# Optimization experiments

Hardware: AMD Instinct MI355X
Metric: run time of the kernel (lower is better)

## Reference

```python
import jax, jax.numpy as jnp
import numpy as np

B, IN, OUT, E, H, K = 8192, 1024, 256, 16, 512, 3
EPS = 1e-10


def setup_inputs() -> dict:
    key = jax.random.key(0)
    ks = jax.random.split(key, 5)
    scaled = lambda k, shape, fan: jax.random.normal(k, shape, jnp.float32) / np.sqrt(fan)
    return {
        "x": jax.random.normal(ks[0], (B, IN), jnp.float32),
        # torch init is zeros for w_gate (degenerate ties); use small random for a meaningful reference
        "w_gate": jax.random.normal(ks[1], (IN, E), jnp.float32) * 0.02,
        "W1": scaled(ks[2], (E, IN, H), IN),
        "b1": jnp.zeros((E, H), jnp.float32),
        "W2": scaled(ks[3], (E, H, OUT), H),
        "b2": jnp.zeros((E, OUT), jnp.float32),
    }


def _cv_squared(v):
    # torch .var() is unbiased (ddof=1)
    return jnp.var(v, ddof=1) / (jnp.mean(v) ** 2 + EPS)


def reference(x, w_gate, W1, b1, W2, b2):
    # --- top-k gating (eval mode: clean logits, no noise) ---
    logits = x @ w_gate                                   # [B, E]
    top_vals, top_idx = jax.lax.top_k(logits, K)          # [B, K]
    top_gates = jax.nn.softmax(top_vals, axis=-1)         # softmax over selected k
    rows = jnp.arange(logits.shape[0])[:, None]
    gates = jnp.zeros_like(logits).at[rows, top_idx].set(top_gates)  # sparse gates [B, E]

    # --- load-balancing loss ---
    importance = gates.sum(0)
    load = (gates > 0).sum(0).astype(jnp.float32)         # _gates_to_load (eval path)
    loss = _cv_squared(importance) + _cv_squared(load)

    # --- experts (MLP stand-in; dense compute, sparse combine via zero gates) ---
    h = jax.nn.relu(jnp.einsum('bi,eih->beh', x, W1) + b1)  # [B, E, H]
    expert_out = jnp.einsum('beh,eho->beo', h, W2) + b2     # [B, E, OUT]

    # combine: equivalent to SparseDispatcher gather/split/scatter-add with gate weighting
    y = jnp.einsum('be,beo->bo', gates, expert_out)         # [B, OUT]
    return y, loss
```

## Files before the change

### kernel.cpp

```cpp
#include <hip/hip_runtime.h>

#define B_ 8192
#define IN_ 1024
#define OUT_ 256
#define E_ 16
#define KTOP 3
#define H_ 512
#define MAXSLOTS 26624
#define NTILES 208
#define HBLK 16

typedef __bf16 bf16;
typedef __bf16 bf16x4 __attribute__((ext_vector_type(4)));
typedef __bf16 bf16x8 __attribute__((ext_vector_type(8)));
typedef float f32x4 __attribute__((ext_vector_type(4)));

__device__ __forceinline__ void async16(const bf16* g, bf16* l) {
    __builtin_amdgcn_global_load_lds(
        (const __attribute__((address_space(1))) void*)g,
        (__attribute__((address_space(3))) void*)l,
        16, 0, 0);
}

__global__ __launch_bounds__(256) void k_setup(
    const float* __restrict__ W1, bf16* __restrict__ w1t,
    const float* __restrict__ W2, bf16* __restrict__ w2t,
    int* __restrict__ row_ids, const float* __restrict__ wg, float* __restrict__ wgT,
    bf16* __restrict__ zero_row, int* __restrict__ tile_expert) {
    int bx = blockIdx.x;
    int t = threadIdx.x;
    if (bx >= 2560) {
        if (bx < 2664) {
            row_ids[(bx - 2560) * 256 + t] = -1;
        } else if (bx < 2728) {
            int id = (bx - 2664) * 256 + t;
            int e = id >> 10, j = id & 1023;
            wgT[id] = wg[j * E_ + e];
        } else {
#pragma unroll
            for (int i = 0; i < 4; i++) zero_row[t * 4 + i] = (bf16)0.f;
            if (t < NTILES) tile_expert[t] = -1;
        }
        return;
    }
    __shared__ float tile[64][65];
    const float* in; bf16* out; int Kd, Nd, e, tk, tn;
    if (bx < 2048) {
        in = W1; out = w1t; Kd = IN_; Nd = H_;
        e = bx >> 7; int tt = bx & 127; tk = tt >> 3; tn = tt & 7;
    } else {
        int b2x = bx - 2048;
        in = W2; out = w2t; Kd = H_; Nd = OUT_;
        e = b2x >> 5; int tt = b2x & 31; tk = tt >> 2; tn = tt & 3;
    }
    int r = t >> 6, c = t & 63;
    const float* src = in + ((size_t)e * Kd + tk * 64) * Nd + (size_t)tn * 64;
#pragma unroll
    for (int i = 0; i < 16; i++) {
        int rr = r + i * 4;
        tile[rr][c] = src[(size_t)rr * Nd + c];
    }
    __syncthreads();
    bf16* dst = out + ((size_t)e * Nd + tn * 64) * Kd + (size_t)tk * 64;
#pragma unroll
    for (int i = 0; i < 16; i++) {
        int rr = r + i * 4;
        dst[(size_t)rr * Kd + c] = (bf16)tile[c][rr];
    }
}

__global__ __launch_bounds__(256) void k_gating(
    const float* __restrict__ x, const float* __restrict__ wgT,
    bf16* __restrict__ xbf, int* __restrict__ top_idx, float* __restrict__ top_gate) {
    int t = threadIdx.x;
    int row = blockIdx.x * 4 + (t >> 6);
    int lane = t & 63;
    float acc[16];
#pragma unroll
    for (int e = 0; e < 16; e++) acc[e] = 0.f;
    const float4* x4p = (const float4*)(x + (size_t)row * IN_);
    const float4* w4 = (const float4*)wgT;
#pragma unroll
    for (int it = 0; it < 4; it++) {
        int j0 = it * 64 + lane;
        float4 xv = x4p[j0];
        bf16x4 xb;
        xb[0] = (bf16)xv.x; xb[1] = (bf16)xv.y; xb[2] = (bf16)xv.z; xb[3] = (bf16)xv.w;
        *(bf16x4*)(xbf + (size_t)row * IN_ + j0 * 4) = xb;
#pragma unroll
        for (int e = 0; e < 16; e++) {
            float4 wv = w4[e * 256 + j0];
            acc[e] += xv.x * wv.x + xv.y * wv.y + xv.z * wv.z + xv.w * wv.w;
        }
    }
#pragma unroll
    for (int e = 0; e < 16; e++) {
#pragma unroll
        for (int s = 32; s > 0; s >>= 1) acc[e] += __shfl_xor(acc[e], s, 64);
    }
    if (lane == 0) {
        float v[16];
#pragma unroll
        for (int e = 0; e < 16; e++) v[e] = acc[e];
        int idx[KTOP];
        float val[KTOP];
#pragma unroll
        for (int k = 0; k < KTOP; k++) {
            int best = 0;
            float bv = v[0];
            for (int e = 1; e < 16; e++) {
                if (v[e] > bv) { bv = v[e]; best = e; }
            }
            idx[k] = best; val[k] = bv; v[best] = -1e30f;
        }
        float e1 = __expf(val[1] - val[0]);
        float e2 = __expf(val[2] - val[0]);
        float inv = 1.f / (1.f + e1 + e2);
        float g[KTOP] = {inv, e1 * inv, e2 * inv};
#pragma unroll
        for (int k = 0; k < KTOP; k++) {
            top_idx[row * KTOP + k] = idx[k];
            top_gate[row * KTOP + k] = g[k];
        }
    }
}

__global__ __launch_bounds__(256) void k_hist(
    const int* __restrict__ top_idx, int* __restrict__ partial) {
    __shared__ int wcnt[4][16];
    int t = threadIdx.x;
    int w = t >> 6, lane = t & 63;
    int blk = blockIdx.x;
    int cnt[16];
#pragma unroll
    for (int k = 0; k < 16; k++) cnt[k] = 0;
#pragma unroll
    for (int j = 0; j < 6; j++) {
        int e = top_idx[blk * 1536 + j * 256 + t];
#pragma unroll
        for (int k = 0; k < 16; k++)
            cnt[k] += (int)__popcll(__ballot(e == k));
    }
    if (lane == 0) {
#pragma unroll
        for (int k = 0; k < 16; k++) wcnt[w][k] = cnt[k];
    }
    __syncthreads();
    if (t < 16) partial[blk * 16 + t] = wcnt[0][t] + wcnt[1][t] + wcnt[2][t] + wcnt[3][t];
}

__global__ __launch_bounds__(256) void k_scan(
    const int* __restrict__ partial, int* __restrict__ counts,
    int* __restrict__ tile_expert, int* __restrict__ gbase) {
    __shared__ int sp[HBLK * 16];
    __shared__ int soff[16];
    int t = threadIdx.x;
    sp[t] = partial[t];
    __syncthreads();
    if (t < 16) {
        int s = 0;
#pragma unroll
        for (int b = 0; b < HBLK; b++) s += sp[b * 16 + t];
        counts[t] = s;
    }
    __syncthreads();
    if (t == 0) {
        int off = 0;
        for (int e = 0; e < E_; e++) {
            int c = 0;
#pragma unroll
            for (int b = 0; b < HBLK; b++) c += sp[b * 16 + e];
            soff[e] = off;
            int pd = (c + 127) & ~127;
            int t0 = off >> 7, t1 = (off + pd) >> 7;
            for (int tt = t0; tt < t1; ++tt) tile_expert[tt] = e;
            off += pd;
        }
    }
    __syncthreads();
    {
        int b = t >> 4, e = t & 15;
        int s = soff[e];
        for (int bp = 0; bp < b; bp++) s += sp[bp * 16 + e];
        gbase[t] = s;
    }
}

__global__ __launch_bounds__(256) void k_scatter(
    const int* __restrict__ top_idx, const float* __restrict__ top_gate,
    const int* __restrict__ gbase,
    int* __restrict__ row_ids, int* __restrict__ rowslot,
    float* __restrict__ partial_imp) {
    __shared__ int lcnt[16];
    __shared__ float limp[16];
    int t = threadIdx.x;
    int blk = blockIdx.x;
    if (t < 16) { lcnt[t] = 0; limp[t] = 0.f; }
    __syncthreads();
#pragma unroll
    for (int j = 0; j < 6; j++) {
        int gid = blk * 1536 + j * 256 + t;
        int e = top_idx[gid];
        float g = top_gate[gid];
        int rank = atomicAdd(&lcnt[e], 1);
        atomicAdd(&limp[e], g);
        int slot = gbase[blk * 16 + e] + rank;
        row_ids[slot] = gid / KTOP;
        rowslot[gid] = slot;
    }
    __syncthreads();
    if (t < 16) partial_imp[blk * 16 + t] = limp[t];
}

__global__ __launch_bounds__(256) void k_gemm1(
    const bf16* __restrict__ xbf, const bf16* __restrict__ w1t,
    const float* __restrict__ b1, const int* __restrict__ row_ids,
    const int* __restrict__ tile_expert, const bf16* __restrict__ zero_row,
    bf16* __restrict__ h) {
    int e = tile_expert[blockIdx.y];
    if (e < 0) return;
    int slot_base = blockIdx.y * 128;
    int nbase = blockIdx.x * 128;
    __shared__ __align__(16) bf16 As[128 * 64];
    __shared__ __align__(16) bf16 Bs[128 * 64];
    int t = threadIdx.x;
    int rmod = (t >> 3) & 7;
    int cglob = (t & 7) ^ rmod;
    const bf16* gA[4];
    const bf16* gB[4];
#pragma unroll
    for (int j = 0; j < 4; j++) {
        int m = j * 32 + (t >> 3);
        int rid = row_ids[slot_base + m];
        gA[j] = ((rid >= 0) ? xbf + (size_t)rid * IN_ : zero_row) + cglob * 8;
        gB[j] = w1t + ((size_t)e * H_ + nbase + m) * IN_ + cglob * 8;
    }
    int w = t >> 6, lane = t & 63;
    int wm = (w >> 1) * 64, wn = (w & 1) * 64;
    int lm = lane & 15, lq = lane >> 4;
    f32x4 acc[4][4] = {};
    for (int k0 = 0; k0 < IN_; k0 += 64) {
#pragma unroll
        for (int j = 0; j < 4; j++) {
            async16(gA[j] + k0, As + (j * 256 + t) * 8);
            async16(gB[j] + k0, Bs + (j * 256 + t) * 8);
        }
        __syncthreads();
        const bf16x8* Av = (const bf16x8*)As;
        const bf16x8* Bv = (const bf16x8*)Bs;
#pragma unroll
        for (int ks = 0; ks < 2; ks++) {
            int kc = ks * 4 + lq;
            bf16x8 af[4], bfv[4];
#pragma unroll
            for (int i = 0; i < 4; i++) {
                int row = wm + i * 16 + lm;
                af[i] = Av[row * 8 + (kc ^ (row & 7))];
            }
#pragma unroll
            for (int i = 0; i < 4; i++) {
                int row = wn + i * 16 + lm;
                bfv[i] = Bv[row * 8 + (kc ^ (row & 7))];
            }
#pragma unroll
            for (int mi = 0; mi < 4; mi++)
#pragma unroll
                for (int ni = 0; ni < 4; ni++)
                    acc[mi][ni] = __builtin_amdgcn_mfma_f32_16x16x32_bf16(af[mi], bfv[ni], acc[mi][ni], 0, 0, 0);
        }
        __syncthreads();
    }
#pragma unroll
    for (int mi = 0; mi < 4; mi++) {
#pragma unroll
        for (int ni = 0; ni < 4; ni++) {
            int colg = nbase + wn + ni * 16 + lm;
            float bias = b1[e * H_ + colg];
#pragma unroll
            for (int r = 0; r < 4; r++) {
                int rowl = wm + mi * 16 + lq * 4 + r;
                float v = acc[mi][ni][r] + bias;
                v = v > 0.f ? v : 0.f;
                h[(size_t)(slot_base + rowl) * H_ + colg] = (bf16)v;
            }
        }
    }
}

__global__ __launch_bounds__(256) void k_gemm2(
    const bf16* __restrict__ h, const bf16* __restrict__ w2t,
    const float* __restrict__ b2, const int* __restrict__ tile_expert,
    bf16* __restrict__ eout) {
    int e = tile_expert[blockIdx.x];
    if (e < 0) return;
    int slot_base = blockIdx.x * 128;
    __shared__ __align__(16) bf16 As[128 * 64];
    __shared__ __align__(16) bf16 Bs[256 * 64];
    int t = threadIdx.x;
    int rmod = (t >> 3) & 7;
    int cglob = (t & 7) ^ rmod;
    const bf16* gA[4];
    const bf16* gB[8];
#pragma unroll
    for (int j = 0; j < 4; j++) {
        int m = j * 32 + (t >> 3);
        gA[j] = h + (size_t)(slot_base + m) * H_ + cglob * 8;
    }
#pragma unroll
    for (int j = 0; j < 8; j++) {
        int m = j * 32 + (t >> 3);
        gB[j] = w2t + ((size_t)e * OUT_ + m) * H_ + cglob * 8;
    }
    int w = t >> 6, lane = t & 63;
    int wm = (w >> 1) * 64, wn = (w & 1) * 128;
    int lm = lane & 15, lq = lane >> 4;
    f32x4 acc[4][8] = {};
    for (int k0 = 0; k0 < H_; k0 += 64) {
#pragma unroll
        for (int j = 0; j < 4; j++) async16(gA[j] + k0, As + (j * 256 + t) * 8);
#pragma unroll
        for (int j = 0; j < 8; j++) async16(gB[j] + k0, Bs + (j * 256 + t) * 8);
        __syncthreads();
        const bf16x8* Av = (const bf16x8*)As;
        const bf16x8* Bv = (const bf16x8*)Bs;
#pragma unroll
        for (int ks = 0; ks < 2; ks++) {
            int kc = ks * 4 + lq;
            bf16x8 af[4], bfv[8];
#pragma unroll
            for (int i = 0; i < 4; i++) {
                int row = wm + i * 16 + lm;
                af[i] = Av[row * 8 + (kc ^ (row & 7))];
            }
#pragma unroll
            for (int i = 0; i < 8; i++) {
                int row = wn + i * 16 + lm;
                bfv[i] = Bv[row * 8 + (kc ^ (row & 7))];
            }
#pragma unroll
            for (int mi = 0; mi < 4; mi++)
#pragma unroll
                for (int ni = 0; ni < 8; ni++)
                    acc[mi][ni] = __builtin_amdgcn_mfma_f32_16x16x32_bf16(af[mi], bfv[ni], acc[mi][ni], 0, 0, 0);
        }
        __syncthreads();
    }
#pragma unroll
    for (int mi = 0; mi < 4; mi++) {
#pragma unroll
        for (int ni = 0; ni < 8; ni++) {
            int colg = wn + ni * 16 + lm;
            float bias = b2[e * OUT_ + colg];
#pragma unroll
            for (int r = 0; r < 4; r++) {
                int rowl = wm + mi * 16 + lq * 4 + r;
                eout[(size_t)(slot_base + rowl) * OUT_ + colg] = (bf16)(acc[mi][ni][r] + bias);
            }
        }
    }
}

__global__ __launch_bounds__(256) void k_combine(
    const bf16* __restrict__ eout, const int* __restrict__ rowslot,
    const float* __restrict__ top_gate, float* __restrict__ y,
    const float* __restrict__ partial_imp, const int* __restrict__ counts,
    float* __restrict__ loss_out) {
    int t = threadIdx.x;
    if (blockIdx.x == B_ / 4) {
        __shared__ float imp[16];
        if (t < 16) {
            float s = 0.f;
#pragma unroll
            for (int b = 0; b < HBLK; b++) s += partial_imp[b * 16 + t];
            imp[t] = s;
        }
        __syncthreads();
        if (t == 0) {
            float si = 0.f, sl = 0.f;
            for (int e = 0; e < E_; e++) { si += imp[e]; sl += (float)counts[e]; }
            float mi_ = si / (float)E_, ml_ = sl / (float)E_;
            float vi = 0.f, vl = 0.f;
            for (int e = 0; e < E_; e++) {
                float d = imp[e] - mi_; vi += d * d;
                float d2 = (float)counts[e] - ml_; vl += d2 * d2;
            }
            vi /= (float)(E_ - 1); vl /= (float)(E_ - 1);
            *loss_out = vi / (mi_ * mi_ + 1e-10f) + vl / (ml_ * ml_ + 1e-10f);
        }
        return;
    }
    int b = blockIdx.x * 4 + (t >> 6);
    int lane = t & 63;
    int s0 = rowslot[b * 3], s1 = rowslot[b * 3 + 1], s2 = rowslot[b * 3 + 2];
    float g0 = top_gate[b * 3], g1 = top_gate[b * 3 + 1], g2 = top_gate[b * 3 + 2];
    bf16x4 v0 = *(const bf16x4*)(eout + (size_t)s0 * OUT_ + lane * 4);
    bf16x4 v1 = *(const bf16x4*)(eout + (size_t)s1 * OUT_ + lane * 4);
    bf16x4 v2 = *(const bf16x4*)(eout + (size_t)s2 * OUT_ + lane * 4);
    float4 r;
    r.x = g0 * (float)v0[0] + g1 * (float)v1[0] + g2 * (float)v2[0];
    r.y = g0 * (float)v0[1] + g1 * (float)v1[1] + g2 * (float)v2[1];
    r.z = g0 * (float)v0[2] + g1 * (float)v1[2] + g2 * (float)v2[2];
    r.w = g0 * (float)v0[3] + g1 * (float)v1[3] + g2 * (float)v2[3];
    ((float4*)y)[(size_t)b * 64 + lane] = r;
}

extern "C" void kernel_launch(void* const* d_in, const int* in_sizes, int n_in,
                              void* d_out, int out_size, void* d_ws, size_t ws_size,
                              hipStream_t stream) {
    (void)in_sizes; (void)n_in; (void)out_size; (void)ws_size;
    const float* x = (const float*)d_in[0];
    const float* wgate = (const float*)d_in[1];
    const float* W1 = (const float*)d_in[2];
    const float* b1 = (const float*)d_in[3];
    const float* W2 = (const float*)d_in[4];
    const float* b2 = (const float*)d_in[5];
    float* y = (float*)d_out;

    char* p = (char*)d_ws;
    auto alloc = [&](size_t bytes) {
        char* q = p;
        p += (bytes + 255) & ~(size_t)255;
        return q;
    };
    bf16* xbf = (bf16*)alloc((size_t)B_ * IN_ * 2);
    bf16* w1t = (bf16*)alloc((size_t)E_ * H_ * IN_ * 2);
    bf16* w2t = (bf16*)alloc((size_t)E_ * OUT_ * H_ * 2);
    bf16* h = (bf16*)alloc((size_t)MAXSLOTS * H_ * 2);
    int* row_ids = (int*)alloc((size_t)MAXSLOTS * 4);
    int* rowslot = (int*)alloc((size_t)B_ * KTOP * 4);
    int* top_idx = (int*)alloc((size_t)B_ * KTOP * 4);
    float* top_gate = (float*)alloc((size_t)B_ * KTOP * 4);
    int* counts = (int*)alloc(E_ * 4);
    int* partial = (int*)alloc(HBLK * E_ * 4);
    int* gbase = (int*)alloc(HBLK * E_ * 4);
    float* partial_imp = (float*)alloc(HBLK * E_ * 4);
    int* tile_expert = (int*)alloc(NTILES * 4);
    bf16* zero_row = (bf16*)alloc(IN_ * 2);
    float* wgT = (float*)alloc((size_t)E_ * IN_ * 4);
    bf16* eout = (bf16*)xbf;

    k_setup<<<dim3(2729), dim3(256), 0, stream>>>(
        W1, w1t, W2, w2t, row_ids, wgate, wgT, zero_row, tile_expert);
    k_gating<<<dim3(B_ / 4), dim3(256), 0, stream>>>(x, wgT, xbf, top_idx, top_gate);
    k_hist<<<dim3(HBLK), dim3(256), 0, stream>>>(top_idx, partial);
    k_scan<<<dim3(1), dim3(256), 0, stream>>>(partial, counts, tile_expert, gbase);
    k_scatter<<<dim3(HBLK), dim3(256), 0, stream>>>(
        top_idx, top_gate, gbase, row_ids, rowslot, partial_imp);
    k_gemm1<<<dim3(H_ / 128, NTILES), dim3(256), 0, stream>>>(
        xbf, w1t, b1, row_ids, tile_expert, zero_row, h);
    k_gemm2<<<dim3(NTILES), dim3(256), 0, stream>>>(
        h, w2t, b2, tile_expert, eout);
    k_combine<<<dim3(B_ / 4 + 1), dim3(256), 0, stream>>>(
        eout, rowslot, top_gate, y, partial_imp, counts, y + (size_t)B_ * OUT_);
}
```

Before: 219.4 us.

## Fuse expert histogram into gating and merge scan with scatter kernel

The gating kernel now counts its own top-k expert assignments in shared memory and writes per-block partial histograms. The separate histogram and single-block scan kernels are removed, and each scatter block recomputes the global prefix offsets and tile-to-expert map from the 2048 partials. This cuts two kernel launches and their serialization, in exchange for redundant prefix work in each of the 16 scatter blocks and shared-memory atomics in gating.

```diff
diff --git a/kernel.cpp b/kernel.cpp
--- a/kernel.cpp
+++ b/kernel.cpp
@@ -9,6 +9,7 @@
 #define MAXSLOTS 26624
 #define NTILES 208
 #define HBLK 16
+#define GBLK 2048
 
 typedef __bf16 bf16;
 typedef __bf16 bf16x4 __attribute__((ext_vector_type(4)));
@@ -71,10 +72,14 @@
 
 __global__ __launch_bounds__(256) void k_gating(
     const float* __restrict__ x, const float* __restrict__ wgT,
-    bf16* __restrict__ xbf, int* __restrict__ top_idx, float* __restrict__ top_gate) {
+    bf16* __restrict__ xbf, int* __restrict__ top_idx, float* __restrict__ top_gate,
+    int* __restrict__ partial) {
+    __shared__ int lcnt[16];
     int t = threadIdx.x;
     int row = blockIdx.x * 4 + (t >> 6);
     int lane = t & 63;
+    if (t < 16) lcnt[t] = 0;
+    __syncthreads();
     float acc[16];
 #pragma unroll
     for (int e = 0; e < 16; e++) acc[e] = 0.f;
@@ -121,90 +126,65 @@
         for (int k = 0; k < KTOP; k++) {
             top_idx[row * KTOP + k] = idx[k];
             top_gate[row * KTOP + k] = g[k];
-        }
-    }
-}
-
-__global__ __launch_bounds__(256) void k_hist(
-    const int* __restrict__ top_idx, int* __restrict__ partial) {
-    __shared__ int wcnt[4][16];
-    int t = threadIdx.x;
-    int w = t >> 6, lane = t & 63;
-    int blk = blockIdx.x;
-    int cnt[16];
-#pragma unroll
-    for (int k = 0; k < 16; k++) cnt[k] = 0;
-#pragma unroll
-    for (int j = 0; j < 6; j++) {
-        int e = top_idx[blk * 1536 + j * 256 + t];
-#pragma unroll
-        for (int k = 0; k < 16; k++)
-            cnt[k] += (int)__popcll(__ballot(e == k));
-    }
-    if (lane == 0) {
-#pragma unroll
-        for (int k = 0; k < 16; k++) wcnt[w][k] = cnt[k];
-    }
-    __syncthreads();
-    if (t < 16) partial[blk * 16 + t] = wcnt[0][t] + wcnt[1][t] + wcnt[2][t] + wcnt[3][t];
-}
-
-__global__ __launch_bounds__(256) void k_scan(
-    const int* __restrict__ partial, int* __restrict__ counts,
-    int* __restrict__ tile_expert, int* __restrict__ gbase) {
-    __shared__ int sp[HBLK * 16];
-    __shared__ int soff[16];
-    int t = threadIdx.x;
-    sp[t] = partial[t];
-    __syncthreads();
-    if (t < 16) {
-        int s = 0;
-#pragma unroll
-        for (int b = 0; b < HBLK; b++) s += sp[b * 16 + t];
-        counts[t] = s;
-    }
-    __syncthreads();
-    if (t == 0) {
-        int off = 0;
-        for (int e = 0; e < E_; e++) {
-            int c = 0;
-#pragma unroll
-            for (int b = 0; b < HBLK; b++) c += sp[b * 16 + e];
-            soff[e] = off;
-            int pd = (c + 127) & ~127;
-            int t0 = off >> 7, t1 = (off + pd) >> 7;
-            for (int tt = t0; tt < t1; ++tt) tile_expert[tt] = e;
-            off += pd;
-        }
-    }
-    __syncthreads();
-    {
-        int b = t >> 4, e = t & 15;
-        int s = soff[e];
-        for (int bp = 0; bp < b; bp++) s += sp[bp * 16 + e];
-        gbase[t] = s;
-    }
-}
-
-__global__ __launch_bounds__(256) void k_scatter(
+            atomicAdd(&lcnt[idx[k]], 1);
+        }
+    }
+    __syncthreads();
+    if (t < 16) partial[blockIdx.x * 16 + t] = lcnt[t];
+}
+
+__global__ __launch_bounds__(256) void k_scatterscan(
     const int* __restrict__ top_idx, const float* __restrict__ top_gate,
-    const int* __restrict__ gbase,
+    const int* __restrict__ partial,
+    int* __restrict__ counts, int* __restrict__ tile_expert,
     int* __restrict__ row_ids, int* __restrict__ rowslot,
     float* __restrict__ partial_imp) {
+    __shared__ int segsum[16][16];
+    __shared__ int tote[16];
+    __shared__ int sbase[16];
     __shared__ int lcnt[16];
     __shared__ float limp[16];
     int t = threadIdx.x;
     int blk = blockIdx.x;
+    int e = t & 15, seg = t >> 4;
+    int s = 0;
+    for (int i = 0; i < 128; i++) s += partial[(seg * 128 + i) * 16 + e];
+    segsum[seg][e] = s;
     if (t < 16) { lcnt[t] = 0; limp[t] = 0.f; }
+    __syncthreads();
+    if (t < 16) {
+        int total = 0, pre = 0;
+        for (int sg = 0; sg < 16; sg++) {
+            int v = segsum[sg][t];
+            total += v;
+            if (sg < blk) pre += v;
+        }
+        tote[t] = total;
+        segsum[0][t] = pre;
+    }
+    __syncthreads();
+    if (t < 16) {
+        int off = 0;
+        for (int ee = 0; ee < 16; ee++) {
+            if (ee == t) break;
+            off += (tote[ee] + 127) & ~127;
+        }
+        sbase[t] = off + segsum[0][t];
+        if (blk == 0) {
+            counts[t] = tote[t];
+            int pd = (tote[t] + 127) & ~127;
+            for (int tt = off >> 7; tt < (off + pd) >> 7; ++tt) tile_expert[tt] = t;
+        }
+    }
     __syncthreads();
 #pragma unroll
     for (int j = 0; j < 6; j++) {
         int gid = blk * 1536 + j * 256 + t;
-        int e = top_idx[gid];
+        int ee = top_idx[gid];
         float g = top_gate[gid];
-        int rank = atomicAdd(&lcnt[e], 1);
-        atomicAdd(&limp[e], g);
-        int slot = gbase[blk * 16 + e] + rank;
+        int rank = atomicAdd(&lcnt[ee], 1);
+        atomicAdd(&limp[ee], g);
+        int slot = sbase[ee] + rank;
         row_ids[slot] = gid / KTOP;
         rowslot[gid] = slot;
     }
@@ -431,8 +411,7 @@
     int* top_idx = (int*)alloc((size_t)B_ * KTOP * 4);
     float* top_gate = (float*)alloc((size_t)B_ * KTOP * 4);
     int* counts = (int*)alloc(E_ * 4);
-    int* partial = (int*)alloc(HBLK * E_ * 4);
-    int* gbase = (int*)alloc(HBLK * E_ * 4);
+    int* partial = (int*)alloc((size_t)GBLK * E_ * 4);
     float* partial_imp = (float*)alloc(HBLK * E_ * 4);
     int* tile_expert = (int*)alloc(NTILES * 4);
     bf16* zero_row = (bf16*)alloc(IN_ * 2);
@@ -441,11 +420,9 @@
 
     k_setup<<<dim3(2729), dim3(256), 0, stream>>>(
         W1, w1t, W2, w2t, row_ids, wgate, wgT, zero_row, tile_expert);
-    k_gating<<<dim3(B_ / 4), dim3(256), 0, stream>>>(x, wgT, xbf, top_idx, top_gate);
-    k_hist<<<dim3(HBLK), dim3(256), 0, stream>>>(top_idx, partial);
-    k_scan<<<dim3(1), dim3(256), 0, stream>>>(partial, counts, tile_expert, gbase);
-    k_scatter<<<dim3(HBLK), dim3(256), 0, stream>>>(
-        top_idx, top_gate, gbase, row_ids, rowslot, partial_imp);
+    k_gating<<<dim3(GBLK), dim3(256), 0, stream>>>(x, wgT, xbf, top_idx, top_gate, partial);
+    k_scatterscan<<<dim3(HBLK), dim3(256), 0, stream>>>(
+        top_idx, top_gate, partial, counts, tile_expert, row_ids, rowslot, partial_imp);
     k_gemm1<<<dim3(H_ / 128, NTILES), dim3(256), 0, stream>>>(
         xbf, w1t, b1, row_ids, tile_expert, zero_row, h);
     k_gemm2<<<dim3(NTILES), dim3(256), 0, stream>>>(
```

Measured after the change: 212.4 us. -3.2%, faster.
